# Kernel tuning notes

Measured on AMD Instinct MI355X. Metric: run time of the kernel, lower is better.

## Reference

```python
import math
import jax, jax.numpy as jnp
import numpy as np

BASE = 10000.0
SCALING_FACTOR = 1.0
ORIG_MAX_POS = 4096
BETA_FAST, BETA_SLOW = 32, 1
MSCALE = 0.707
MSCALE_ALL_DIM = 0.707


def _yarn_cos_sin(seq_len: int, dim: int):
    # DeepseekV3YarnRotaryEmbedding._set_cos_sin_cache, computed in numpy (constants)
    def corr_dim(num_rot):
        return dim * math.log(ORIG_MAX_POS / (num_rot * 2 * math.pi)) / (2 * math.log(BASE))
    low = max(math.floor(corr_dim(BETA_FAST)), 0)
    high = min(math.ceil(corr_dim(BETA_SLOW)), dim - 1)
    hi = high + 0.001 if low == high else high
    ramp = np.clip((np.arange(dim // 2, dtype=np.float32) - low) / (hi - low), 0.0, 1.0)
    inv_freq_mask = 1.0 - ramp
    freq_extra = 1.0 / BASE ** (np.arange(0, dim, 2, dtype=np.float32) / dim)
    freq_inter = freq_extra / SCALING_FACTOR
    inv_freq = freq_inter * (1.0 - inv_freq_mask) + freq_extra * inv_freq_mask
    t = np.arange(seq_len, dtype=np.float32)
    freqs = np.outer(t, inv_freq)
    def get_mscale(s, m):
        return 1.0 if s <= 1 else 0.1 * m * math.log(s) + 1.0
    _m = get_mscale(SCALING_FACTOR, MSCALE) / get_mscale(SCALING_FACTOR, MSCALE_ALL_DIM)
    emb = np.concatenate([freqs, freqs], axis=-1)  # [S, dim]
    return jnp.asarray(np.cos(emb) * _m), jnp.asarray(np.sin(emb) * _m)


def _rotate_half(x):
    x1, x2 = jnp.split(x, 2, axis=-1)
    return jnp.concatenate([-x2, x1], axis=-1)


def setup_inputs() -> dict:
    key = jax.random.key(0)
    ks = jax.random.split(key, 5)
    B, S, H, DN, DR, DV = 2, 2048, 16, 128, 64, 128
    return {
        "q_nope": jax.random.normal(ks[0], (B, S, H, DN), jnp.float32),
        "q_pe": jax.random.normal(ks[1], (B, S, H, DR), jnp.float32),
        "k_nope": jax.random.normal(ks[2], (B, S, H, DN), jnp.float32),
        "k_pe": jax.random.normal(ks[3], (B, S, 1, DR), jnp.float32),  # shared rope key head
        "v": jax.random.normal(ks[4], (B, S, H, DV), jnp.float32),
    }


def reference(q_nope, q_pe, k_nope, k_pe, v):
    B, S, H, DN = q_nope.shape
    DR = q_pe.shape[-1]
    sm_scale = (DN + DR) ** (-0.5)  # qk_head_dim**-0.5
    cos, sin = _yarn_cos_sin(S, DR)  # [S, DR]
    cos = cos[None, :, None, :]
    sin = sin[None, :, None, :]
    # decoupled RoPE on the rope slice (apply_rotary_pos_emb with position_ids=arange)
    qp = q_pe * cos + _rotate_half(q_pe) * sin              # [B,S,H,DR]
    kp = k_pe * cos + _rotate_half(k_pe) * sin              # [B,S,1,DR]
    kp = jnp.broadcast_to(kp, (B, S, H, DR))
    q = jnp.concatenate([q_nope, qp], axis=-1)              # [B,S,H,DN+DR]
    k = jnp.concatenate([k_nope, kp], axis=-1)
    # attention_ref: full fp32 logits, causal mask, lse*log2(e), softmax, PV
    logits = jnp.einsum('bmhd,bnhd->bhmn', q.astype(jnp.float32), k.astype(jnp.float32)) * sm_scale
    mask = jnp.arange(S)[:, None] >= jnp.arange(S)[None, :]  # qo_len == kv_len
    logits = jnp.where(mask[None, None], logits, -jnp.inf)
    lse = jnp.transpose(jax.scipy.special.logsumexp(logits, axis=-1), (0, 2, 1)) * math.log2(math.e)
    p = jax.nn.softmax(logits, axis=-1)
    o = jnp.einsum('bhmn,bnhd->bmhd', p, v.astype(jnp.float32))
    o = o.reshape(B * S, H, -1).astype(q_nope.dtype)        # [B*S, H, DV]
    return o, lse
```

## Files before the change

kernel.cpp:

```cpp
#include <hip/hip_runtime.h>
#include <hip/hip_bf16.h>
#include <math.h>

#define NB 2
#define SEQ 2048
#define NH 16
#define DNOPE 128
#define DROT 64
#define DVDIM 128
#define DQK 192
#define BM 64
#define BN 64

typedef __bf16 bf16x8_t __attribute__((ext_vector_type(8)));
typedef float f32x4_t __attribute__((ext_vector_type(4)));

#define LOG2_BASE_OVER_HALFDIM 0.41524101186092028f
#define KSL2 0.10412340175817158f

#define KBF_ELEMS   ((size_t)NB * NH * SEQ * DQK)
#define KPREP_BLOCKS 6144
#define VPREP_BLOCKS 1024

__global__ __launch_bounds__(256) void prep_kernel(
    const float* __restrict__ k_nope, const float* __restrict__ k_pe,
    const float* __restrict__ v, __bf16* __restrict__ Kbf,
    __bf16* __restrict__ Vtb) {
  __shared__ __bf16 T[64][130];
  const int bid = blockIdx.x;
  const int tid = threadIdx.x;
  if (bid < KPREP_BLOCKS) {
    int gid = bid * 256 + tid;
    size_t o8 = (size_t)gid * 8;
    int d0 = (int)(o8 % DQK);
    int rest = (int)(o8 / DQK);
    int s = rest & (SEQ - 1);
    int bh = rest >> 11;
    int h = bh & (NH - 1), b = bh >> 4;
    bf16x8_t o;
    if (d0 < DNOPE) {
      const float* p = k_nope + ((size_t)((b * SEQ + s) * NH + h)) * DNOPE + d0;
      float4 a = *(const float4*)p;
      float4 c = *(const float4*)(p + 4);
      o[0] = (__bf16)a.x; o[1] = (__bf16)a.y; o[2] = (__bf16)a.z; o[3] = (__bf16)a.w;
      o[4] = (__bf16)c.x; o[5] = (__bf16)c.y; o[6] = (__bf16)c.z; o[7] = (__bf16)c.w;
    } else {
      int dr0 = d0 - DNOPE;
      const float* p = k_pe + (size_t)(b * SEQ + s) * DROT;
#pragma unroll
      for (int j = 0; j < 8; ++j) {
        int dr = dr0 + j;
        int i = dr & 31;
        float invf = exp2f(-LOG2_BASE_OVER_HALFDIM * (float)i);
        float ang = (float)s * invf;
        float sn, cs; sincosf(ang, &sn, &cs);
        float x = p[dr];
        float oth = (dr < 32) ? -p[dr + 32] : p[dr - 32];
        o[j] = (__bf16)(x * cs + oth * sn);
      }
    }
    *(bf16x8_t*)&Kbf[o8] = o;
  } else {
    int vb = bid - KPREP_BLOCKS;
    const int s0 = (vb & 31) * 64, h = (vb >> 5) & (NH - 1), b = vb >> 9;
#pragma unroll
    for (int r = 0; r < 8; ++r) {
      int task = tid + r * 256;
      int srow = task >> 5, c4 = (task & 31) * 4;
      const float* p = v + ((size_t)((b * SEQ + s0 + srow) * NH + h)) * DVDIM + c4;
      float4 a = *(const float4*)p;
      T[srow][c4 + 0] = (__bf16)a.x; T[srow][c4 + 1] = (__bf16)a.y;
      T[srow][c4 + 2] = (__bf16)a.z; T[srow][c4 + 3] = (__bf16)a.w;
    }
    __syncthreads();
#pragma unroll
    for (int r = 0; r < 4; ++r) {
      int task = tid + r * 256;
      int dv = task >> 3, c8 = (task & 7) * 8;
      bf16x8_t o;
#pragma unroll
      for (int u = 0; u < 8; ++u) o[u] = T[c8 + u][dv];
      *(bf16x8_t*)&Vtb[((size_t)(b * NH + h) * DVDIM + dv) * SEQ + s0 + c8] = o;
    }
  }
}

__global__ __launch_bounds__(256, 2) void mla_fwd_kernel(
    const float* __restrict__ q_nope, const float* __restrict__ q_pe,
    const __bf16* __restrict__ Kbf, const __bf16* __restrict__ Vtb,
    float* __restrict__ out_o, float* __restrict__ out_lse) {
  __shared__ __bf16 Kl[BN * DQK];
  __shared__ __bf16 Vl[DVDIM * BN];
  __shared__ __bf16 Pl[4 * 16 * BN];
  __shared__ __bf16 Vx[16 * 72];

  const int bx = blockIdx.x, h = blockIdx.y, b = blockIdx.z;
  const int tid = threadIdx.x;
  const int w = tid >> 6, lane = tid & 63;
  const int col = lane & 15, quad = lane >> 4;
  const int swz = col & 7;
  const int e0 = quad ^ swz, e1 = (quad + 4) ^ swz;

  for (int i = tid; i < 16 * 72; i += 256)
    Vx[i] = (i < 64) ? (__bf16)1.0f : (__bf16)0.0f;

  const __bf16* Kslab = Kbf + (size_t)(b * NH + h) * SEQ * DQK;
  const __bf16* Vslab = Vtb + (size_t)(b * NH + h) * DVDIM * SEQ;

  int kofs[6];
#pragma unroll
  for (int r = 0; r < 6; ++r) {
    int L = r * 256 + tid;
    int n = L / 24, jj = L - n * 24;
    int jsrc = (jj & ~7) | ((jj & 7) ^ (n & 7));
    kofs[r] = n * DQK + jsrc * 8;
  }
  int vofs[4];
#pragma unroll
  for (int r = 0; r < 4; ++r) {
    int L = r * 256 + tid;
    int dv = L >> 3, jj = L & 7;
    vofs[r] = dv * SEQ + (jj ^ (dv & 7)) * 8;
  }

  __syncthreads();
  const bf16x8_t vxf0 = *(const bf16x8_t*)&Vx[col * 72 + quad * 8];
  const bf16x8_t vxf1 = *(const bf16x8_t*)&Vx[col * 72 + 32 + quad * 8];

  for (int half = 0; half < 2; ++half) {
    const int qt = half ? bx : (31 - bx);
    const int qb = qt * BM;
    const int mrow = qb + w * 16 + col;

    const float* qn = q_nope + (size_t)((b * SEQ + mrow) * NH + h) * DNOPE;
    const float* qp = q_pe   + (size_t)((b * SEQ + mrow) * NH + h) * DROT;
    bf16x8_t qfrag[6];
#pragma unroll
    for (int c = 0; c < 4; ++c) {
      const float* p = qn + c * 32 + quad * 8;
      float4 a = *(const float4*)p;
      float4 bq = *(const float4*)(p + 4);
      bf16x8_t f;
      f[0]=(__bf16)(a.x*KSL2);  f[1]=(__bf16)(a.y*KSL2);
      f[2]=(__bf16)(a.z*KSL2);  f[3]=(__bf16)(a.w*KSL2);
      f[4]=(__bf16)(bq.x*KSL2); f[5]=(__bf16)(bq.y*KSL2);
      f[6]=(__bf16)(bq.z*KSL2); f[7]=(__bf16)(bq.w*KSL2);
      qfrag[c] = f;
    }
    {
      const float* plo = qp + quad * 8;
      const float* phi = qp + 32 + quad * 8;
      float4 lo0 = *(const float4*)plo;
      float4 lo1 = *(const float4*)(plo + 4);
      float4 hi0 = *(const float4*)phi;
      float4 hi1 = *(const float4*)(phi + 4);
      float xl[8] = {lo0.x,lo0.y,lo0.z,lo0.w,lo1.x,lo1.y,lo1.z,lo1.w};
      float xh[8] = {hi0.x,hi0.y,hi0.z,hi0.w,hi1.x,hi1.y,hi1.z,hi1.w};
      bf16x8_t f4v, f5v;
#pragma unroll
      for (int j = 0; j < 8; ++j) {
        int i = quad * 8 + j;
        float invf = exp2f(-LOG2_BASE_OVER_HALFDIM * (float)i);
        float ang = (float)mrow * invf;
        float sn, cs; sincosf(ang, &sn, &cs);
        f4v[j] = (__bf16)((xl[j] * cs - xh[j] * sn) * KSL2);
        f5v[j] = (__bf16)((xh[j] * cs + xl[j] * sn) * KSL2);
      }
      qfrag[4] = f4v; qfrag[5] = f5v;
    }

    f32x4_t oacc[8];
#pragma unroll
    for (int i = 0; i < 8; ++i) oacc[i] = (f32x4_t){0.f, 0.f, 0.f, 0.f};
    f32x4_t lacc = (f32x4_t){0.f, 0.f, 0.f, 0.f};
    float m_run[4] = {-INFINITY, -INFINITY, -INFINITY, -INFINITY};

    bf16x8_t Kreg[6], Vreg[4];
#pragma unroll
    for (int r = 0; r < 6; ++r) Kreg[r] = *(const bf16x8_t*)(Kslab + kofs[r]);
#pragma unroll
    for (int r = 0; r < 4; ++r) Vreg[r] = *(const bf16x8_t*)(Vslab + vofs[r]);

    for (int it = 0; it <= qt; ++it) {
      __syncthreads();
#pragma unroll
      for (int r = 0; r < 6; ++r) *(bf16x8_t*)&Kl[(r * 256 + tid) * 8] = Kreg[r];
#pragma unroll
      for (int r = 0; r < 4; ++r) *(bf16x8_t*)&Vl[(r * 256 + tid) * 8] = Vreg[r];
      __syncthreads();
      if (it < qt) {
        const __bf16* Ksrc = Kslab + (size_t)(it + 1) * BN * DQK;
        const __bf16* Vsrc = Vslab + (it + 1) * BN;
#pragma unroll
        for (int r = 0; r < 6; ++r) Kreg[r] = *(const bf16x8_t*)(Ksrc + kofs[r]);
#pragma unroll
        for (int r = 0; r < 4; ++r) Vreg[r] = *(const bf16x8_t*)(Vsrc + vofs[r]);
      }

      f32x4_t sacc[4];
#pragma unroll
      for (int t = 0; t < 4; ++t) sacc[t] = (f32x4_t){0.f, 0.f, 0.f, 0.f};
#pragma unroll
      for (int t = 0; t < 4; ++t) {
        const __bf16* kr = &Kl[(t * 16 + col) * 24 * 8];
        sacc[t] = __builtin_amdgcn_mfma_f32_16x16x32_bf16(qfrag[0], *(const bf16x8_t*)&kr[e0 * 8], sacc[t], 0, 0, 0);
        sacc[t] = __builtin_amdgcn_mfma_f32_16x16x32_bf16(qfrag[1], *(const bf16x8_t*)&kr[e1 * 8], sacc[t], 0, 0, 0);
        sacc[t] = __builtin_amdgcn_mfma_f32_16x16x32_bf16(qfrag[2], *(const bf16x8_t*)&kr[64 + e0 * 8], sacc[t], 0, 0, 0);
        sacc[t] = __builtin_amdgcn_mfma_f32_16x16x32_bf16(qfrag[3], *(const bf16x8_t*)&kr[64 + e1 * 8], sacc[t], 0, 0, 0);
        sacc[t] = __builtin_amdgcn_mfma_f32_16x16x32_bf16(qfrag[4], *(const bf16x8_t*)&kr[128 + e0 * 8], sacc[t], 0, 0, 0);
        sacc[t] = __builtin_amdgcn_mfma_f32_16x16x32_bf16(qfrag[5], *(const bf16x8_t*)&kr[128 + e1 * 8], sacc[t], 0, 0, 0);
      }

      const bool diag = (it == qt);
      float pv[4][4];
      float alpha[4];
#pragma unroll
      for (int r = 0; r < 4; ++r) {
        float mx = -INFINITY;
#pragma unroll
        for (int t = 0; t < 4; ++t) {
          float sv = sacc[t][r];
          if (diag) {
            int nn = (qt << 6) + t * 16 + col;
            int mm = qb + w * 16 + quad * 4 + r;
            if (nn > mm) sv = -INFINITY;
          }
          pv[t][r] = sv;
          mx = fmaxf(mx, sv);
        }
        mx = fmaxf(mx, __shfl_xor(mx, 1, 64));
        mx = fmaxf(mx, __shfl_xor(mx, 2, 64));
        mx = fmaxf(mx, __shfl_xor(mx, 4, 64));
        mx = fmaxf(mx, __shfl_xor(mx, 8, 64));
        float mnew = fmaxf(m_run[r], mx);
        alpha[r] = exp2f(m_run[r] - mnew);
        m_run[r] = mnew;
#pragma unroll
        for (int t = 0; t < 4; ++t) pv[t][r] = exp2f(pv[t][r] - mnew);
      }
#pragma unroll
      for (int d = 0; d < 8; ++d) {
        f32x4_t o = oacc[d];
        o[0] *= alpha[0]; o[1] *= alpha[1]; o[2] *= alpha[2]; o[3] *= alpha[3];
        oacc[d] = o;
      }
      lacc[0] *= alpha[0]; lacc[1] *= alpha[1];
      lacc[2] *= alpha[2]; lacc[3] *= alpha[3];

      __bf16* Pw = &Pl[w * 16 * BN];
#pragma unroll
      for (int t = 0; t < 4; ++t)
#pragma unroll
        for (int r = 0; r < 4; ++r) {
          int row = quad * 4 + r;
          int j = t * 2 + (col >> 3);
          Pw[(row * 8 + (j ^ (row & 7))) * 8 + (col & 7)] = (__bf16)pv[t][r];
        }
      bf16x8_t pf0 = *(const bf16x8_t*)&Pw[(col * 8 + e0) * 8];
      bf16x8_t pf1 = *(const bf16x8_t*)&Pw[(col * 8 + e1) * 8];

#pragma unroll
      for (int d = 0; d < 8; ++d) {
        const __bf16* vr = &Vl[(d * 16 + col) * 64];
        bf16x8_t vf0 = *(const bf16x8_t*)&vr[e0 * 8];
        bf16x8_t vf1 = *(const bf16x8_t*)&vr[e1 * 8];
        oacc[d] = __builtin_amdgcn_mfma_f32_16x16x32_bf16(pf0, vf0, oacc[d], 0, 0, 0);
        oacc[d] = __builtin_amdgcn_mfma_f32_16x16x32_bf16(pf1, vf1, oacc[d], 0, 0, 0);
      }
      lacc = __builtin_amdgcn_mfma_f32_16x16x32_bf16(pf0, vxf0, lacc, 0, 0, 0);
      lacc = __builtin_amdgcn_mfma_f32_16x16x32_bf16(pf1, vxf1, lacc, 0, 0, 0);
    }

    float lr[4];
#pragma unroll
    for (int r = 0; r < 4; ++r) lr[r] = __shfl(lacc[r], lane & 48, 64);
    float inv_l[4];
#pragma unroll
    for (int r = 0; r < 4; ++r) inv_l[r] = 1.0f / lr[r];
#pragma unroll
    for (int d = 0; d < 8; ++d) {
#pragma unroll
      for (int r = 0; r < 4; ++r) {
        int mm = qb + w * 16 + quad * 4 + r;
        out_o[(size_t)((b * SEQ + mm) * NH + h) * DVDIM + d * 16 + col] = oacc[d][r] * inv_l[r];
      }
    }
    if (col < 4) {
      int r = col;
      int mm = qb + w * 16 + quad * 4 + r;
      out_lse[(size_t)(b * SEQ + mm) * NH + h] = m_run[r] + log2f(lr[r]);
    }
  }
}

extern "C" void kernel_launch(void* const* d_in, const int* in_sizes, int n_in,
                              void* d_out, int out_size, void* d_ws, size_t ws_size,
                              hipStream_t stream) {
  const float* q_nope = (const float*)d_in[0];
  const float* q_pe   = (const float*)d_in[1];
  const float* k_nope = (const float*)d_in[2];
  const float* k_pe   = (const float*)d_in[3];
  const float* v      = (const float*)d_in[4];
  float* out_o   = (float*)d_out;
  float* out_lse = out_o + (size_t)NB * SEQ * NH * DVDIM;

  __bf16* Kbf = (__bf16*)d_ws;
  __bf16* Vtb = Kbf + KBF_ELEMS;

  prep_kernel<<<dim3(KPREP_BLOCKS + VPREP_BLOCKS), dim3(256), 0, stream>>>(
      k_nope, k_pe, v, Kbf, Vtb);
  mla_fwd_kernel<<<dim3(16, NH, NB), dim3(256), 0, stream>>>(
      q_nope, q_pe, Kbf, Vtb, out_o, out_lse);
}
```

Measured before the change: 264.2 us.

## Double-buffer K in LDS via direct global-to-LDS loads, read V straight from global

Replaces the register-staged K/V prefetch with asynchronous global_load_lds writes into two ping-ponged K buffers, cutting one barrier per iteration and register pressure. V fragments are now loaded directly from global memory into registers per tile instead of via LDS. It also swaps sincosf for a range-reduced hardware sin/cos intrinsic in the RoPE paths. The risks are uncoalesced or strided V global reads and exposed load latency, since V is fetched in the same iteration it is used. The hardware sin/cos adds a small accuracy risk.

New measurement: 321.6 us. 21.8% more time.

```diff
diff --git a/kernel.cpp b/kernel.cpp
--- a/kernel.cpp
+++ b/kernel.cpp
@@ -17,10 +17,26 @@
 
 #define LOG2_BASE_OVER_HALFDIM 0.41524101186092028f
 #define KSL2 0.10412340175817158f
+#define INV2PI 0.15915494309189535f
 
 #define KBF_ELEMS   ((size_t)NB * NH * SEQ * DQK)
 #define KPREP_BLOCKS 6144
 #define VPREP_BLOCKS 1024
+
+__device__ __forceinline__ void fast_sincos(float ang, float* sn, float* cs) {
+  float rev = ang * INV2PI;
+  float r = rev - rintf(rev);
+  *sn = __builtin_amdgcn_sinf(r);
+  *cs = __builtin_amdgcn_cosf(r);
+}
+
+__device__ __forceinline__ void load_lds16(const __bf16* g, __bf16* l) {
+  __builtin_amdgcn_global_load_lds(
+      (const __attribute__((address_space(1))) unsigned int*)g,
+      (__attribute__((address_space(3))) unsigned int*)l, 16, 0, 0);
+}
+
+#define WAIT_VM0() __builtin_amdgcn_s_waitcnt(0x0F70)
 
 __global__ __launch_bounds__(256) void prep_kernel(
     const float* __restrict__ k_nope, const float* __restrict__ k_pe,
@@ -52,8 +68,8 @@
         int dr = dr0 + j;
         int i = dr & 31;
         float invf = exp2f(-LOG2_BASE_OVER_HALFDIM * (float)i);
-        float ang = (float)s * invf;
-        float sn, cs; sincosf(ang, &sn, &cs);
+        float sn, cs;
+        fast_sincos((float)s * invf, &sn, &cs);
         float x = p[dr];
         float oth = (dr < 32) ? -p[dr + 32] : p[dr - 32];
         o[j] = (__bf16)(x * cs + oth * sn);
@@ -89,9 +105,9 @@
     const float* __restrict__ q_nope, const float* __restrict__ q_pe,
     const __bf16* __restrict__ Kbf, const __bf16* __restrict__ Vtb,
     float* __restrict__ out_o, float* __restrict__ out_lse) {
-  __shared__ __bf16 Kl[BN * DQK];
-  __shared__ __bf16 Vl[DVDIM * BN];
-  __shared__ __bf16 Pl[4 * 16 * BN];
+  __shared__ __bf16 KlA[BN * DQK];
+  __shared__ __bf16 KlB[BN * DQK];
+  __shared__ __bf16 Pl[4][16 * BN];
   __shared__ __bf16 Vx[16 * 72];
 
   const int bx = blockIdx.x, h = blockIdx.y, b = blockIdx.z;
@@ -100,6 +116,7 @@
   const int col = lane & 15, quad = lane >> 4;
   const int swz = col & 7;
   const int e0 = quad ^ swz, e1 = (quad + 4) ^ swz;
+  const int wo = w * 512;
 
   for (int i = tid; i < 16 * 72; i += 256)
     Vx[i] = (i < 64) ? (__bf16)1.0f : (__bf16)0.0f;
@@ -115,13 +132,6 @@
     int jsrc = (jj & ~7) | ((jj & 7) ^ (n & 7));
     kofs[r] = n * DQK + jsrc * 8;
   }
-  int vofs[4];
-#pragma unroll
-  for (int r = 0; r < 4; ++r) {
-    int L = r * 256 + tid;
-    int dv = L >> 3, jj = L & 7;
-    vofs[r] = dv * SEQ + (jj ^ (dv & 7)) * 8;
-  }
 
   __syncthreads();
   const bf16x8_t vxf0 = *(const bf16x8_t*)&Vx[col * 72 + quad * 8];
@@ -131,6 +141,12 @@
     const int qt = half ? bx : (31 - bx);
     const int qb = qt * BM;
     const int mrow = qb + w * 16 + col;
+
+    WAIT_VM0();
+    __syncthreads();
+#pragma unroll
+    for (int r = 0; r < 6; ++r)
+      load_lds16(Kslab + kofs[r], &KlA[r * 2048 + wo]);
 
     const float* qn = q_nope + (size_t)((b * SEQ + mrow) * NH + h) * DNOPE;
     const float* qp = q_pe   + (size_t)((b * SEQ + mrow) * NH + h) * DROT;
@@ -161,8 +177,8 @@
       for (int j = 0; j < 8; ++j) {
         int i = quad * 8 + j;
         float invf = exp2f(-LOG2_BASE_OVER_HALFDIM * (float)i);
-        float ang = (float)mrow * invf;
-        float sn, cs; sincosf(ang, &sn, &cs);
+        float sn, cs;
+        fast_sincos((float)mrow * invf, &sn, &cs);
         f4v[j] = (__bf16)((xl[j] * cs - xh[j] * sn) * KSL2);
         f5v[j] = (__bf16)((xh[j] * cs + xl[j] * sn) * KSL2);
       }
@@ -175,34 +191,29 @@
     f32x4_t lacc = (f32x4_t){0.f, 0.f, 0.f, 0.f};
     float m_run[4] = {-INFINITY, -INFINITY, -INFINITY, -INFINITY};
 
-    bf16x8_t Kreg[6], Vreg[4];
-#pragma unroll
-    for (int r = 0; r < 6; ++r) Kreg[r] = *(const bf16x8_t*)(Kslab + kofs[r]);
-#pragma unroll
-    for (int r = 0; r < 4; ++r) Vreg[r] = *(const bf16x8_t*)(Vslab + vofs[r]);
-
-    for (int it = 0; it <= qt; ++it) {
+    auto phase = [&](const __bf16* Kc, __bf16* Kn, int it) {
+      WAIT_VM0();
       __syncthreads();
-#pragma unroll
-      for (int r = 0; r < 6; ++r) *(bf16x8_t*)&Kl[(r * 256 + tid) * 8] = Kreg[r];
-#pragma unroll
-      for (int r = 0; r < 4; ++r) *(bf16x8_t*)&Vl[(r * 256 + tid) * 8] = Vreg[r];
-      __syncthreads();
-      if (it < qt) {
-        const __bf16* Ksrc = Kslab + (size_t)(it + 1) * BN * DQK;
-        const __bf16* Vsrc = Vslab + (it + 1) * BN;
-#pragma unroll
-        for (int r = 0; r < 6; ++r) Kreg[r] = *(const bf16x8_t*)(Ksrc + kofs[r]);
-#pragma unroll
-        for (int r = 0; r < 4; ++r) Vreg[r] = *(const bf16x8_t*)(Vsrc + vofs[r]);
-      }
+      const int nt = (it + 1 <= qt) ? it + 1 : qt;
+      const __bf16* Ks = Kslab + (size_t)nt * BN * DQK;
+#pragma unroll
+      for (int r = 0; r < 6; ++r) load_lds16(Ks + kofs[r], &Kn[r * 2048 + wo]);
+
+      const int kb = it * BN;
+      bf16x8_t vf[8][2];
+#pragma unroll
+      for (int d = 0; d < 8; ++d)
+#pragma unroll
+        for (int c = 0; c < 2; ++c)
+          vf[d][c] = *(const bf16x8_t*)(Vslab + (size_t)(d * 16 + col) * SEQ +
+                                        kb + c * 32 + quad * 8);
 
       f32x4_t sacc[4];
 #pragma unroll
       for (int t = 0; t < 4; ++t) sacc[t] = (f32x4_t){0.f, 0.f, 0.f, 0.f};
 #pragma unroll
       for (int t = 0; t < 4; ++t) {
-        const __bf16* kr = &Kl[(t * 16 + col) * 24 * 8];
+        const __bf16* kr = &Kc[(t * 16 + col) * DQK];
         sacc[t] = __builtin_amdgcn_mfma_f32_16x16x32_bf16(qfrag[0], *(const bf16x8_t*)&kr[e0 * 8], sacc[t], 0, 0, 0);
         sacc[t] = __builtin_amdgcn_mfma_f32_16x16x32_bf16(qfrag[1], *(const bf16x8_t*)&kr[e1 * 8], sacc[t], 0, 0, 0);
         sacc[t] = __builtin_amdgcn_mfma_f32_16x16x32_bf16(qfrag[2], *(const bf16x8_t*)&kr[64 + e0 * 8], sacc[t], 0, 0, 0);
@@ -221,7 +232,7 @@
         for (int t = 0; t < 4; ++t) {
           float sv = sacc[t][r];
           if (diag) {
-            int nn = (qt << 6) + t * 16 + col;
+            int nn = kb + t * 16 + col;
             int mm = qb + w * 16 + quad * 4 + r;
             if (nn > mm) sv = -INFINITY;
           }
@@ -247,7 +258,7 @@
       lacc[0] *= alpha[0]; lacc[1] *= alpha[1];
       lacc[2] *= alpha[2]; lacc[3] *= alpha[3];
 
-      __bf16* Pw = &Pl[w * 16 * BN];
+      __bf16* Pw = Pl[w];
 #pragma unroll
       for (int t = 0; t < 4; ++t)
 #pragma unroll
@@ -261,14 +272,16 @@
 
 #pragma unroll
       for (int d = 0; d < 8; ++d) {
-        const __bf16* vr = &Vl[(d * 16 + col) * 64];
-        bf16x8_t vf0 = *(const bf16x8_t*)&vr[e0 * 8];
-        bf16x8_t vf1 = *(const bf16x8_t*)&vr[e1 * 8];
-        oacc[d] = __builtin_amdgcn_mfma_f32_16x16x32_bf16(pf0, vf0, oacc[d], 0, 0, 0);
-        oacc[d] = __builtin_amdgcn_mfma_f32_16x16x32_bf16(pf1, vf1, oacc[d], 0, 0, 0);
+        oacc[d] = __builtin_amdgcn_mfma_f32_16x16x32_bf16(pf0, vf[d][0], oacc[d], 0, 0, 0);
+        oacc[d] = __builtin_amdgcn_mfma_f32_16x16x32_bf16(pf1, vf[d][1], oacc[d], 0, 0, 0);
       }
       lacc = __builtin_amdgcn_mfma_f32_16x16x32_bf16(pf0, vxf0, lacc, 0, 0, 0);
       lacc = __builtin_amdgcn_mfma_f32_16x16x32_bf16(pf1, vxf1, lacc, 0, 0, 0);
+    };
+
+    for (int it = 0; it <= qt; ++it) {
+      if ((it & 1) == 0) phase(KlA, KlB, it);
+      else               phase(KlB, KlA, it);
     }
 
     float lr[4];
```
